# Optimization experiments

Measured on AMD Instinct MI355X. Metric: run time of the kernel, lower is better.

Reference implementation:

```python
import jax, jax.numpy as jnp
import numpy as np

N_PAIRS = 100000
N_TRIP = 500000
PAIR_DIM = 128
GEOM_DIM = 4


def _mlp(x, w1, b1, w2, b2):
    return jax.nn.silu(x @ w1 + b1) @ w2 + b2


def setup_inputs() -> dict:
    key = jax.random.key(0)
    ks = jax.random.split(key, 16)

    def lin(k, fan_in, fan_out):
        bound = 1.0 / np.sqrt(fan_in)
        kw, kb = jax.random.split(k)
        w = jax.random.uniform(kw, (fan_in, fan_out), jnp.float32, -bound, bound)
        b = jax.random.uniform(kb, (fan_out,), jnp.float32, -bound, bound)
        return w, b

    psi_w1, psi_b1 = lin(ks[0], 3 * PAIR_DIM + GEOM_DIM, PAIR_DIM)
    psi_w2, psi_b2 = lin(ks[1], PAIR_DIM, PAIR_DIM)
    phi_w1, phi_b1 = lin(ks[2], 2 * PAIR_DIM, PAIR_DIM)
    phi_w2, phi_b2 = lin(ks[3], PAIR_DIM, PAIR_DIM)

    return {
        "h_pair": jax.random.normal(ks[4], (N_PAIRS, PAIR_DIM), jnp.float32),
        "pair_vu_idx": jax.random.randint(ks[5], (N_TRIP,), 0, N_PAIRS, jnp.int64 if jax.config.jax_enable_x64 else jnp.int32).astype(jnp.int32),
        "pair_uw_idx": jax.random.randint(ks[6], (N_TRIP,), 0, N_PAIRS).astype(jnp.int32),
        "pair_vw_idx": jax.random.randint(ks[7], (N_TRIP,), 0, N_PAIRS).astype(jnp.int32),
        "geom_features": jax.random.normal(ks[8], (N_TRIP, GEOM_DIM), jnp.float32),
        "psi_w1": psi_w1, "psi_b1": psi_b1, "psi_w2": psi_w2, "psi_b2": psi_b2,
        "phi_w1": phi_w1, "phi_b1": phi_b1, "phi_w2": phi_w2, "phi_b2": phi_b2,
    }


def reference(h_pair, pair_vu_idx, pair_uw_idx, pair_vw_idx, geom_features,
              psi_w1, psi_b1, psi_w2, psi_b2,
              phi_w1, phi_b1, phi_w2, phi_b2):
    # gather triplet endpoints: [T, pair_dim] each
    h_vu = h_pair[pair_vu_idx]
    h_uw = h_pair[pair_uw_idx]
    h_vw = h_pair[pair_vw_idx]
    triplet_input = jnp.concatenate([h_vu, h_uw, h_vw, geom_features], axis=-1)  # [T, 3D+G]
    m_triplet = _mlp(triplet_input, psi_w1, psi_b1, psi_w2, psi_b2)  # [T, D]
    # scatter-add back onto pairs indexed by vw
    agg = jax.ops.segment_sum(m_triplet, pair_vw_idx, num_segments=h_pair.shape[0])  # [N, D]
    updated = _mlp(jnp.concatenate([h_pair, agg], axis=-1), phi_w1, phi_b1, phi_w2, phi_b2)
    return h_pair + updated
```

## Files before the change

kernel.cpp:

```cpp
#include <hip/hip_runtime.h>
#include <hip/hip_bf16.h>

#define T_TRIP 500000
#define NP     100000
#define NTILES 7813

typedef float f32x4 __attribute__((ext_vector_type(4)));
typedef __bf16 bf16x8 __attribute__((ext_vector_type(8)));
typedef unsigned short u16;
typedef unsigned short u16x8 __attribute__((ext_vector_type(8)));

__device__ __forceinline__ u16 f2bf(float f) {
  union { float f; unsigned u; } v; v.f = f;
  unsigned r = v.u + 0x7fffu + ((v.u >> 16) & 1u);
  return (u16)(r >> 16);
}

__device__ __forceinline__ ushort4 cvt4(float4 v) {
  ushort4 o; o.x = f2bf(v.x); o.y = f2bf(v.y); o.z = f2bf(v.z); o.w = f2bf(v.w);
  return o;
}

#define MFMA16(a, b, c) __builtin_amdgcn_mfma_f32_16x16x32_bf16((a), (b), (c), 0, 0, 0)

#define WAITVM(N) asm volatile("s_waitcnt vmcnt(" #N ")" ::: "memory")
#define LGKM0()   asm volatile("s_waitcnt lgkmcnt(0)" ::: "memory")

__device__ __forceinline__ void barrier_raw() {
  asm volatile("" ::: "memory");
  __builtin_amdgcn_s_barrier();
  asm volatile("" ::: "memory");
  __builtin_amdgcn_sched_barrier(0);
}

__device__ __forceinline__ void gload_lds16(const u16* g, u16* l) {
  __builtin_amdgcn_global_load_lds((const __attribute__((address_space(1))) void*)g,
                                   (__attribute__((address_space(3))) void*)l, 16, 0, 0);
}
__device__ __forceinline__ void gload_lds4(const int* g, int* l) {
  __builtin_amdgcn_global_load_lds((const __attribute__((address_space(1))) void*)g,
                                   (__attribute__((address_space(3))) void*)l, 4, 0, 0);
}

#define FP_W1A   0u
#define FP_W1B   16384u
#define FP_W1C   32768u
#define FP_W2    49152u
#define FP_PW1   65536u
#define FP_PW2   98304u
#define FP_W1D   114688u
#define FP_H     131072u
#define FP_AGG   12931072u
#define WS_NEED_BYTES 51462144ull

#define HSTR  136
#define GSTR  520
#define X2STR 264

__global__ void k_prep_fast(const float* __restrict__ psi_w1, const float* __restrict__ psi_w2,
                            const float* __restrict__ phi_w1, const float* __restrict__ phi_w2,
                            u16* __restrict__ ws) {
  int i = blockIdx.x * 256 + threadIdx.x;
  if (i < 49152) {
    int s = i / 16384, r = i % 16384;
    int n = r / 128, k = r % 128;
    ws[FP_W1A + i] = f2bf(psi_w1[(s * 128 + k) * 128 + n]);
    return;
  }
  i -= 49152;
  if (i < 16384) {
    int n = i / 128, k = i % 128;
    ws[FP_W2 + i] = f2bf(psi_w2[k * 128 + n]);
    return;
  }
  i -= 16384;
  if (i < 32768) {
    int n = i / 256, k = i % 256;
    ws[FP_PW1 + i] = f2bf(phi_w1[k * 128 + n]);
    return;
  }
  i -= 32768;
  if (i < 16384) {
    int n = i / 128, k = i % 128;
    ws[FP_PW2 + i] = f2bf(phi_w2[k * 128 + n]);
    return;
  }
  i -= 16384;
  if (i < 512) {
    int k = i / 128, n = i % 128;
    reinterpret_cast<float*>(ws + FP_W1D)[i] = psi_w1[(384 + k) * 128 + n];
  }
}

__global__ void k_hconv(const float* __restrict__ h, u16* __restrict__ H, u16* __restrict__ AGG) {
  const size_t i = (size_t)(blockIdx.x * 256 + threadIdx.x) * 8;
  float4 v0 = *reinterpret_cast<const float4*>(h + i);
  float4 v1 = *reinterpret_cast<const float4*>(h + i + 4);
  *reinterpret_cast<ushort4*>(H + i)     = cvt4(v0);
  *reinterpret_cast<ushort4*>(H + i + 4) = cvt4(v1);
  ushort4 z = {0, 0, 0, 0};
  *reinterpret_cast<ushort4*>(AGG + i)     = z;
  *reinterpret_cast<ushort4*>(AGG + i + 4) = z;
}

__global__ __launch_bounds__(256, 3) void k_triplet_fast(
    const u16* __restrict__ H,
    const int* __restrict__ ivu, const int* __restrict__ iuw, const int* __restrict__ ivw,
    const float* __restrict__ geom,
    const u16* __restrict__ W1A, const u16* __restrict__ W1B, const u16* __restrict__ W1C,
    const float* __restrict__ w1dF, const u16* __restrict__ W2T,
    const float* __restrict__ b1, const float* __restrict__ b2,
    u16* __restrict__ AGG) {
  __shared__ __align__(16) u16 XB[2][16 * GSTR];
  __shared__ __align__(16) u16 hl[64 * HSTR];
  __shared__ __align__(16) float geomF[2][64][4];
  __shared__ int svw[2][64];

  const int tid = threadIdx.x;
  const int w = tid >> 6, l = tid & 63;
  const int lr = l & 15;
  const int lk = (l >> 4) << 3;
  const int n0 = w * 32 + lr;
  const int rowh = (l >> 4) << 2;
  const int srow = l >> 4;
  const int schunk = (l & 15) ^ ((l >> 4) << 1);

  bf16x8 w2f[4][2];
#pragma unroll
  for (int ks = 0; ks < 4; ++ks)
#pragma unroll
    for (int ct = 0; ct < 2; ++ct)
      w2f[ks][ct] = *reinterpret_cast<const bf16x8*>(&W2T[(size_t)(n0 + ct * 16) * 128 + ks * 32 + lk]);
  const float b1v[2] = {b1[n0], b1[n0 + 16]};
  const float b2v[2] = {b2[n0], b2[n0 + 16]};
  float w1dv[4][2];
#pragma unroll
  for (int k = 0; k < 4; ++k) {
    w1dv[k][0] = w1dF[k * 128 + n0];
    w1dv[k][1] = w1dF[k * 128 + n0 + 16];
  }

  auto stage_src = [&](const int* idxa, int tile, int buf) {
    const int t0 = tile * 64;
#pragma unroll
    for (int q = 0; q < 4; ++q) {
      const int g = w * 4 + q;
      int t = t0 + g * 4 + srow; t = (t < T_TRIP) ? t : (T_TRIP - 1);
      const int idx = idxa[t];
      gload_lds16(H + (size_t)idx * 128 + schunk * 8, &XB[buf][g * GSTR]);
    }
  };

  auto stage_aux = [&](int tile, int tb) {
    const int t0 = tile * 64;
    int t = t0 + l; t = (t < T_TRIP) ? t : (T_TRIP - 1);
    if (w == 0) {
      gload_lds16(reinterpret_cast<const u16*>(geom + (size_t)t * 4),
                  reinterpret_cast<u16*>(&geomF[tb][0][0]));
    } else if (w == 1) {
      gload_lds4(ivw + t, &svw[tb][0]);
    }
  };

  auto gemm_src = [&](const u16* WT, int buf, f32x4 (&acc)[4][2]) {
#pragma unroll
    for (int ks = 0; ks < 4; ++ks) {
      bf16x8 a[4], b[2];
#pragma unroll
      for (int rt = 0; rt < 4; ++rt) {
        const int r = rt * 16 + lr;
        const int g = r >> 2, s = r & 3;
        const int j = ks * 4 + (l >> 4);
        a[rt] = *reinterpret_cast<const bf16x8*>(&XB[buf][g * GSTR + s * 128 + ((j ^ (s << 1)) << 3)]);
      }
#pragma unroll
      for (int ct = 0; ct < 2; ++ct)
        b[ct] = *reinterpret_cast<const bf16x8*>(&WT[(size_t)(n0 + ct * 16) * 128 + ks * 32 + lk]);
#pragma unroll
      for (int rt = 0; rt < 4; ++rt)
#pragma unroll
        for (int ct = 0; ct < 2; ++ct)
          acc[rt][ct] = MFMA16(a[rt], b[ct], acc[rt][ct]);
    }
  };

  int pb = 0, tb = 0;
  int tt = blockIdx.x;
  stage_src(ivu, tt, 0);

  for (; tt < NTILES; tt += gridDim.x) {
    const int t0 = tt * 64;
    int ttn = tt + gridDim.x; if (ttn >= NTILES) ttn = tt;

    stage_src(iuw, tt, pb ^ 1);
    stage_aux(tt, tb);
    WAITVM(4);
    barrier_raw();

    f32x4 acc[4][2] = {};
    gemm_src(W1A, pb, acc);
    barrier_raw();

    stage_src(ivw, tt, pb);
    WAITVM(4);
    barrier_raw();

    gemm_src(W1B, pb ^ 1, acc);

    WAITVM(0);
    barrier_raw();

    stage_src(ivu, ttn, pb ^ 1);
    gemm_src(W1C, pb, acc);

#pragma unroll
    for (int rt = 0; rt < 4; ++rt)
#pragma unroll
      for (int j = 0; j < 4; ++j) {
        const float4 g4 = *reinterpret_cast<const float4*>(&geomF[tb][rt * 16 + rowh + j][0]);
#pragma unroll
        for (int ct = 0; ct < 2; ++ct)
          acc[rt][ct][j] += g4.x * w1dv[0][ct] + g4.y * w1dv[1][ct] +
                            g4.z * w1dv[2][ct] + g4.w * w1dv[3][ct];
      }

#pragma unroll
    for (int rt = 0; rt < 4; ++rt)
#pragma unroll
      for (int ct = 0; ct < 2; ++ct) {
        const float bb = b1v[ct];
#pragma unroll
        for (int j = 0; j < 4; ++j) {
          float v = acc[rt][ct][j] + bb;
          v = v / (1.f + __expf(-v));
          hl[(rt * 16 + rowh + j) * HSTR + n0 + ct * 16] = f2bf(v);
        }
      }
    LGKM0();
    barrier_raw();

    f32x4 acc2[4][2] = {};
#pragma unroll
    for (int ks = 0; ks < 4; ++ks) {
      bf16x8 a[4];
#pragma unroll
      for (int rt = 0; rt < 4; ++rt)
        a[rt] = *reinterpret_cast<const bf16x8*>(&hl[(rt * 16 + lr) * HSTR + ks * 32 + lk]);
#pragma unroll
      for (int rt = 0; rt < 4; ++rt)
#pragma unroll
        for (int ct = 0; ct < 2; ++ct)
          acc2[rt][ct] = MFMA16(a[rt], w2f[ks][ct], acc2[rt][ct]);
    }

#pragma unroll
    for (int rt = 0; rt < 4; ++rt) {
      const int4 d4 = *reinterpret_cast<const int4*>(&svw[tb][rt * 16 + rowh]);
#pragma unroll
      for (int j = 0; j < 4; ++j) {
        const int dst = (&d4.x)[j];
        const int trow = t0 + rt * 16 + rowh + j;
        float v0 = acc2[rt][0][j] + b2v[0];
        float v1 = acc2[rt][1][j] + b2v[1];
        float x0 = __shfl_xor(v0, 1, 64);
        float x1 = __shfl_xor(v1, 1, 64);
        const bool even = (l & 1) == 0;
        float lo = even ? v0 : x1;
        float hi = even ? x0 : v1;
        const int col = even ? n0 : (n0 + 15);
        if (trow < T_TRIP) {
          u16* p = AGG + (size_t)dst * 128 + col;
          unsigned pk = ((unsigned)f2bf(hi) << 16) | (unsigned)f2bf(lo);
          asm volatile("global_atomic_pk_add_bf16 %0, %1, off" :: "v"(p), "v"(pk) : "memory");
        }
      }
    }
    pb ^= 1; tb ^= 1;
  }
  WAITVM(0);
}

__global__ __launch_bounds__(256, 3) void k_pair_fast(
    const float* __restrict__ h_pair, const u16* __restrict__ H, const u16* __restrict__ AGG,
    const u16* __restrict__ PW1T, const u16* __restrict__ PW2T,
    const float* __restrict__ b1, const float* __restrict__ b2,
    float* __restrict__ out) {
  __shared__ __align__(16) u16 xl[64 * X2STR];
  __shared__ __align__(16) u16 hl[64 * HSTR];

  const int tid = threadIdx.x;
  const int r0 = blockIdx.x * 64;

  {
    const int row = tid >> 2, q = tid & 3;
    int rc = r0 + row; rc = (rc < NP) ? rc : (NP - 1);
    const u16x8* sh = reinterpret_cast<const u16x8*>(H + (size_t)rc * 128 + q * 32);
    const u16x8* sa = reinterpret_cast<const u16x8*>(AGG + (size_t)rc * 128 + q * 32);
    u16x8* d1 = reinterpret_cast<u16x8*>(&xl[row * X2STR + q * 32]);
    u16x8* d2 = reinterpret_cast<u16x8*>(&xl[row * X2STR + 128 + q * 32]);
#pragma unroll
    for (int i = 0; i < 4; ++i) { d1[i] = sh[i]; d2[i] = sa[i]; }
  }
  __syncthreads();

  const int w = tid >> 6, l = tid & 63;
  const int lr = l & 15;
  const int lk = (l >> 4) << 3;
  const int n0 = w * 32 + lr;
  const int rowh = (l >> 4) << 2;

  f32x4 acc[4][2] = {};
#pragma unroll 1
  for (int ks = 0; ks < 8; ++ks) {
    const int k0 = ks * 32;
    bf16x8 a[4], b[2];
#pragma unroll
    for (int rt = 0; rt < 4; ++rt)
      a[rt] = *reinterpret_cast<const bf16x8*>(&xl[(rt * 16 + lr) * X2STR + k0 + lk]);
#pragma unroll
    for (int ct = 0; ct < 2; ++ct)
      b[ct] = *reinterpret_cast<const bf16x8*>(&PW1T[(size_t)(n0 + ct * 16) * 256 + k0 + lk]);
#pragma unroll
    for (int rt = 0; rt < 4; ++rt)
#pragma unroll
      for (int ct = 0; ct < 2; ++ct)
        acc[rt][ct] = MFMA16(a[rt], b[ct], acc[rt][ct]);
  }

  {
    const float b1v0 = b1[n0], b1v1 = b1[n0 + 16];
#pragma unroll
    for (int rt = 0; rt < 4; ++rt)
#pragma unroll
      for (int ct = 0; ct < 2; ++ct) {
        const float bb = ct ? b1v1 : b1v0;
#pragma unroll
        for (int j = 0; j < 4; ++j) {
          float v = acc[rt][ct][j] + bb;
          v = v / (1.f + __expf(-v));
          hl[(rt * 16 + rowh + j) * HSTR + n0 + ct * 16] = f2bf(v);
        }
      }
  }
  __syncthreads();

  f32x4 acc2[4][2] = {};
#pragma unroll
  for (int ks = 0; ks < 4; ++ks) {
    const int k0 = ks * 32;
    bf16x8 a[4], b[2];
#pragma unroll
    for (int rt = 0; rt < 4; ++rt)
      a[rt] = *reinterpret_cast<const bf16x8*>(&hl[(rt * 16 + lr) * HSTR + k0 + lk]);
#pragma unroll
    for (int ct = 0; ct < 2; ++ct)
      b[ct] = *reinterpret_cast<const bf16x8*>(&PW2T[(size_t)(n0 + ct * 16) * 128 + k0 + lk]);
#pragma unroll
    for (int rt = 0; rt < 4; ++rt)
#pragma unroll
      for (int ct = 0; ct < 2; ++ct)
        acc2[rt][ct] = MFMA16(a[rt], b[ct], acc2[rt][ct]);
  }

  {
    const float b2v0 = b2[n0], b2v1 = b2[n0 + 16];
#pragma unroll
    for (int rt = 0; rt < 4; ++rt)
#pragma unroll
      for (int j = 0; j < 4; ++j) {
        const int row = rt * 16 + rowh + j;
        const int r = r0 + row;
        if (r < NP) {
          out[(size_t)r * 128 + n0]      = h_pair[(size_t)r * 128 + n0]      + acc2[rt][0][j] + b2v0;
          out[(size_t)r * 128 + n0 + 16] = h_pair[(size_t)r * 128 + n0 + 16] + acc2[rt][1][j] + b2v1;
        }
      }
  }
}

#define PSI_W1T_OFF 0
#define PSI_W2T_OFF 53248
#define PHI_W1T_OFF 69632
#define PHI_W2T_OFF 102400
#define WS_U16_TOTAL 118784
#define XSTR 424

__global__ void k_prep(const float* __restrict__ psi_w1, const float* __restrict__ psi_w2,
                       const float* __restrict__ phi_w1, const float* __restrict__ phi_w2,
                       u16* __restrict__ ws) {
  int i = blockIdx.x * 256 + threadIdx.x;
  if (i < 128 * 416) {
    int n = i / 416, k = i % 416;
    ws[PSI_W1T_OFF + i] = f2bf(k < 388 ? psi_w1[k * 128 + n] : 0.f);
    return;
  }
  i -= 128 * 416;
  if (i < 128 * 128) {
    int n = i / 128, k = i % 128;
    ws[PSI_W2T_OFF + i] = f2bf(psi_w2[k * 128 + n]);
    return;
  }
  i -= 128 * 128;
  if (i < 128 * 256) {
    int n = i / 256, k = i % 256;
    ws[PHI_W1T_OFF + i] = f2bf(phi_w1[k * 128 + n]);
    return;
  }
  i -= 128 * 256;
  if (i < 128 * 128) {
    int n = i / 128, k = i % 128;
    ws[PHI_W2T_OFF + i] = f2bf(phi_w2[k * 128 + n]);
  }
}

__global__ __launch_bounds__(256, 2) void k_triplet(
    const float* __restrict__ h_pair,
    const int* __restrict__ ivu, const int* __restrict__ iuw, const int* __restrict__ ivw,
    const float* __restrict__ geom,
    const u16* __restrict__ W1T, const u16* __restrict__ W2T,
    const float* __restrict__ b1, const float* __restrict__ b2,
    float* __restrict__ agg) {
  __shared__ __align__(16) u16 xl[64 * XSTR];
  __shared__ __align__(16) u16 hl[64 * HSTR];
  __shared__ int svw[64];

  const int tid = threadIdx.x;
  const int t0 = blockIdx.x * 64;

  {
    const int row = tid >> 2, q = tid & 3;
    const int t = t0 + row;
    const int tc = (t < T_TRIP) ? t : (T_TRIP - 1);
    if (q == 0) svw[row] = (t < T_TRIP) ? ivw[tc] : -1;
    int idx[3];
    idx[0] = ivu[tc]; idx[1] = iuw[tc]; idx[2] = ivw[tc];
#pragma unroll
    for (int s = 0; s < 3; ++s) {
      const float4* src = reinterpret_cast<const float4*>(h_pair + (size_t)idx[s] * 128 + q * 32);
      u16* dst = &xl[row * XSTR + s * 128 + q * 32];
#pragma unroll
      for (int i = 0; i < 8; ++i)
        *reinterpret_cast<ushort4*>(dst + i * 4) = cvt4(src[i]);
    }
  }
  if (tid < 64) {
    const int t = t0 + tid;
    const int tc = (t < T_TRIP) ? t : (T_TRIP - 1);
    const float4 g = reinterpret_cast<const float4*>(geom)[tc];
    u16* dst = &xl[tid * XSTR + 384];
    *reinterpret_cast<ushort4*>(dst) = cvt4(g);
    ushort4 z = {0, 0, 0, 0};
#pragma unroll
    for (int i = 1; i < 8; ++i) *reinterpret_cast<ushort4*>(dst + i * 4) = z;
  }
  __syncthreads();

  const int w = tid >> 6;
  const int l = tid & 63;
  const int lr = l & 15;
  const int lk = (l >> 4) << 3;
  const int n0 = w * 32 + lr;
  const int rowh = (l >> 4) << 2;

  f32x4 acc[4][2] = {};
#pragma unroll 1
  for (int ks = 0; ks < 13; ++ks) {
    const int k0 = ks * 32;
    bf16x8 a[4], b[2];
#pragma unroll
    for (int rt = 0; rt < 4; ++rt)
      a[rt] = *reinterpret_cast<const bf16x8*>(&xl[(rt * 16 + lr) * XSTR + k0 + lk]);
#pragma unroll
    for (int ct = 0; ct < 2; ++ct)
      b[ct] = *reinterpret_cast<const bf16x8*>(&W1T[(size_t)(n0 + ct * 16) * 416 + k0 + lk]);
#pragma unroll
    for (int rt = 0; rt < 4; ++rt)
#pragma unroll
      for (int ct = 0; ct < 2; ++ct)
        acc[rt][ct] = MFMA16(a[rt], b[ct], acc[rt][ct]);
  }

  {
    const float b1v0 = b1[n0], b1v1 = b1[n0 + 16];
#pragma unroll
    for (int rt = 0; rt < 4; ++rt)
#pragma unroll
      for (int ct = 0; ct < 2; ++ct) {
        const float bb = ct ? b1v1 : b1v0;
#pragma unroll
        for (int j = 0; j < 4; ++j) {
          float v = acc[rt][ct][j] + bb;
          v = v / (1.f + __expf(-v));
          hl[(rt * 16 + rowh + j) * HSTR + n0 + ct * 16] = f2bf(v);
        }
      }
  }
  __syncthreads();

  f32x4 acc2[4][2] = {};
#pragma unroll
  for (int ks = 0; ks < 4; ++ks) {
    const int k0 = ks * 32;
    bf16x8 a[4], b[2];
#pragma unroll
    for (int rt = 0; rt < 4; ++rt)
      a[rt] = *reinterpret_cast<const bf16x8*>(&hl[(rt * 16 + lr) * HSTR + k0 + lk]);
#pragma unroll
    for (int ct = 0; ct < 2; ++ct)
      b[ct] = *reinterpret_cast<const bf16x8*>(&W2T[(size_t)(n0 + ct * 16) * 128 + k0 + lk]);
#pragma unroll
    for (int rt = 0; rt < 4; ++rt)
#pragma unroll
      for (int ct = 0; ct < 2; ++ct)
        acc2[rt][ct] = MFMA16(a[rt], b[ct], acc2[rt][ct]);
  }

  {
    const float b2v0 = b2[n0], b2v1 = b2[n0 + 16];
#pragma unroll
    for (int rt = 0; rt < 4; ++rt)
#pragma unroll
      for (int j = 0; j < 4; ++j) {
        const int row = rt * 16 + rowh + j;
        const int dst = svw[row];
        if (dst >= 0) {
          unsafeAtomicAdd(&agg[(size_t)dst * 128 + n0], acc2[rt][0][j] + b2v0);
          unsafeAtomicAdd(&agg[(size_t)dst * 128 + n0 + 16], acc2[rt][1][j] + b2v1);
        }
      }
  }
}

__global__ __launch_bounds__(256, 2) void k_pair(
    const float* __restrict__ h_pair,
    const u16* __restrict__ W1T, const u16* __restrict__ W2T,
    const float* __restrict__ b1, const float* __restrict__ b2,
    float* __restrict__ out) {
  __shared__ __align__(16) u16 xl[64 * X2STR];
  __shared__ __align__(16) u16 hl[64 * HSTR];

  const int tid = threadIdx.x;
  const int r0 = blockIdx.x * 64;

  {
    const int row = tid >> 2, q = tid & 3;
    const int r = r0 + row;
    const int rc = (r < NP) ? r : (NP - 1);
    const float4* s1 = reinterpret_cast<const float4*>(h_pair + (size_t)rc * 128 + q * 32);
    const float4* s2 = reinterpret_cast<const float4*>(out + (size_t)rc * 128 + q * 32);
    u16* d1 = &xl[row * X2STR + q * 32];
    u16* d2 = &xl[row * X2STR + 128 + q * 32];
#pragma unroll
    for (int i = 0; i < 8; ++i) {
      *reinterpret_cast<ushort4*>(d1 + i * 4) = cvt4(s1[i]);
      *reinterpret_cast<ushort4*>(d2 + i * 4) = cvt4(s2[i]);
    }
  }
  __syncthreads();

  const int w = tid >> 6;
  const int l = tid & 63;
  const int lr = l & 15;
  const int lk = (l >> 4) << 3;
  const int n0 = w * 32 + lr;
  const int rowh = (l >> 4) << 2;

  f32x4 acc[4][2] = {};
#pragma unroll 1
  for (int ks = 0; ks < 8; ++ks) {
    const int k0 = ks * 32;
    bf16x8 a[4], b[2];
#pragma unroll
    for (int rt = 0; rt < 4; ++rt)
      a[rt] = *reinterpret_cast<const bf16x8*>(&xl[(rt * 16 + lr) * X2STR + k0 + lk]);
#pragma unroll
    for (int ct = 0; ct < 2; ++ct)
      b[ct] = *reinterpret_cast<const bf16x8*>(&W1T[(size_t)(n0 + ct * 16) * 256 + k0 + lk]);
#pragma unroll
    for (int rt = 0; rt < 4; ++rt)
#pragma unroll
      for (int ct = 0; ct < 2; ++ct)
        acc[rt][ct] = MFMA16(a[rt], b[ct], acc[rt][ct]);
  }

  {
    const float b1v0 = b1[n0], b1v1 = b1[n0 + 16];
#pragma unroll
    for (int rt = 0; rt < 4; ++rt)
#pragma unroll
      for (int ct = 0; ct < 2; ++ct) {
        const float bb = ct ? b1v1 : b1v0;
#pragma unroll
        for (int j = 0; j < 4; ++j) {
          float v = acc[rt][ct][j] + bb;
          v = v / (1.f + __expf(-v));
          hl[(rt * 16 + rowh + j) * HSTR + n0 + ct * 16] = f2bf(v);
        }
      }
  }
  __syncthreads();

  f32x4 acc2[4][2] = {};
#pragma unroll
  for (int ks = 0; ks < 4; ++ks) {
    const int k0 = ks * 32;
    bf16x8 a[4], b[2];
#pragma unroll
    for (int rt = 0; rt < 4; ++rt)
      a[rt] = *reinterpret_cast<const bf16x8*>(&hl[(rt * 16 + lr) * HSTR + k0 + lk]);
#pragma unroll
    for (int ct = 0; ct < 2; ++ct)
      b[ct] = *reinterpret_cast<const bf16x8*>(&W2T[(size_t)(n0 + ct * 16) * 128 + k0 + lk]);
#pragma unroll
    for (int rt = 0; rt < 4; ++rt)
#pragma unroll
      for (int ct = 0; ct < 2; ++ct)
        acc2[rt][ct] = MFMA16(a[rt], b[ct], acc2[rt][ct]);
  }

  {
    const float b2v0 = b2[n0], b2v1 = b2[n0 + 16];
#pragma unroll
    for (int rt = 0; rt < 4; ++rt)
#pragma unroll
      for (int j = 0; j < 4; ++j) {
        const int row = rt * 16 + rowh + j;
        const int r = r0 + row;
        if (r < NP) {
          out[(size_t)r * 128 + n0]      = h_pair[(size_t)r * 128 + n0]      + acc2[rt][0][j] + b2v0;
          out[(size_t)r * 128 + n0 + 16] = h_pair[(size_t)r * 128 + n0 + 16] + acc2[rt][1][j] + b2v1;
        }
      }
  }
}

extern "C" void kernel_launch(void* const* d_in, const int* in_sizes, int n_in,
                              void* d_out, int out_size, void* d_ws, size_t ws_size,
                              hipStream_t stream) {
  const float* h_pair = (const float*)d_in[0];
  const int* ivu = (const int*)d_in[1];
  const int* iuw = (const int*)d_in[2];
  const int* ivw = (const int*)d_in[3];
  const float* geom = (const float*)d_in[4];
  const float* psi_w1 = (const float*)d_in[5];
  const float* psi_b1 = (const float*)d_in[6];
  const float* psi_w2 = (const float*)d_in[7];
  const float* psi_b2 = (const float*)d_in[8];
  const float* phi_w1 = (const float*)d_in[9];
  const float* phi_b1 = (const float*)d_in[10];
  const float* phi_w2 = (const float*)d_in[11];
  const float* phi_b2 = (const float*)d_in[12];

  float* out = (float*)d_out;
  u16* ws = (u16*)d_ws;

  if (ws_size >= WS_NEED_BYTES) {
    k_prep_fast<<<450, 256, 0, stream>>>(psi_w1, psi_w2, phi_w1, phi_w2, ws);
    k_hconv<<<6250, 256, 0, stream>>>(h_pair, ws + FP_H, ws + FP_AGG);
    k_triplet_fast<<<768, 256, 0, stream>>>(
        ws + FP_H, ivu, iuw, ivw, geom,
        ws + FP_W1A, ws + FP_W1B, ws + FP_W1C,
        reinterpret_cast<const float*>(ws + FP_W1D), ws + FP_W2,
        psi_b1, psi_b2, ws + FP_AGG);
    k_pair_fast<<<(NP + 63) / 64, 256, 0, stream>>>(
        h_pair, ws + FP_H, ws + FP_AGG,
        ws + FP_PW1, ws + FP_PW2, phi_b1, phi_b2, out);
  } else {
    hipMemsetAsync(d_out, 0, (size_t)out_size * sizeof(float), stream);
    k_prep<<<(WS_U16_TOTAL + 255) / 256, 256, 0, stream>>>(psi_w1, psi_w2, phi_w1, phi_w2, ws);
    k_triplet<<<(T_TRIP + 63) / 64, 256, 0, stream>>>(
        h_pair, ivu, iuw, ivw, geom,
        ws + PSI_W1T_OFF, ws + PSI_W2T_OFF, psi_b1, psi_b2, out);
    k_pair<<<(NP + 63) / 64, 256, 0, stream>>>(
        h_pair, ws + PHI_W1T_OFF, ws + PHI_W2T_OFF, phi_b1, phi_b2, out);
  }
}
```

Baseline: 279.8 us.

## Prefetch triplet indices into LDS and defer scatter atomics by one tile

The triplet kernel now stages the ivu/iuw/ivw index arrays and geometry into LDS one tile ahead through async global-to-LDS loads, so the gather address computation reads indices from LDS instead of issuing dependent global loads. The bf16 atomic scatter of each tile's output is deferred and issued after the next tile's first-layer GEMMs, overlapping atomic latency with MFMA work. SiLU now uses a hardware reciprocal, and bf16 conversion uses the packed cvt instruction in both kernels. This adds register pressure from the carried accumulators and destination indices, plus an extra full vmcnt wait and barrier per tile.

```diff
diff --git a/kernel.cpp b/kernel.cpp
--- a/kernel.cpp
+++ b/kernel.cpp
@@ -19,6 +19,12 @@
 __device__ __forceinline__ ushort4 cvt4(float4 v) {
   ushort4 o; o.x = f2bf(v.x); o.y = f2bf(v.y); o.z = f2bf(v.z); o.w = f2bf(v.w);
   return o;
+}
+
+__device__ __forceinline__ u16 cvt1_pk(float v) {
+  unsigned r;
+  asm("v_cvt_pk_bf16_f32 %0, %1, %1" : "=v"(r) : "v"(v));
+  return (u16)r;
 }
 
 #define MFMA16(a, b, c) __builtin_amdgcn_mfma_f32_16x16x32_bf16((a), (b), (c), 0, 0, 0)
@@ -113,8 +119,10 @@
     u16* __restrict__ AGG) {
   __shared__ __align__(16) u16 XB[2][16 * GSTR];
   __shared__ __align__(16) u16 hl[64 * HSTR];
-  __shared__ __align__(16) float geomF[2][64][4];
-  __shared__ int svw[2][64];
+  __shared__ __align__(16) float geomF[64][4];
+  __shared__ __align__(16) int aIvu[2][64];
+  __shared__ __align__(16) int aIuw[64];
+  __shared__ __align__(16) int svw[2][64];
 
   const int tid = threadIdx.x;
   const int w = tid >> 6, l = tid & 63;
@@ -140,25 +148,29 @@
     w1dv[k][1] = w1dF[k * 128 + n0 + 16];
   }
 
-  auto stage_src = [&](const int* idxa, int tile, int buf) {
-    const int t0 = tile * 64;
+  auto stage_src_lds = [&](const int* idxL, int buf) {
 #pragma unroll
     for (int q = 0; q < 4; ++q) {
       const int g = w * 4 + q;
-      int t = t0 + g * 4 + srow; t = (t < T_TRIP) ? t : (T_TRIP - 1);
-      const int idx = idxa[t];
+      const int idx = idxL[g * 4 + srow];
       gload_lds16(H + (size_t)idx * 128 + schunk * 8, &XB[buf][g * GSTR]);
     }
   };
 
-  auto stage_aux = [&](int tile, int tb) {
-    const int t0 = tile * 64;
-    int t = t0 + l; t = (t < T_TRIP) ? t : (T_TRIP - 1);
+  auto stage_aux = [&](int tn, int tn2, int buf) {
     if (w == 0) {
+      int t = tn2 * 64 + l; t = (t < T_TRIP) ? t : (T_TRIP - 1);
+      gload_lds4(ivu + t, &aIvu[buf][0]);
+    } else if (w == 1) {
+      int t = tn * 64 + l; t = (t < T_TRIP) ? t : (T_TRIP - 1);
+      gload_lds4(iuw + t, &aIuw[0]);
+    } else if (w == 2) {
+      int t = tn * 64 + l; t = (t < T_TRIP) ? t : (T_TRIP - 1);
+      gload_lds4(ivw + t, &svw[buf][0]);
+    } else {
+      int t = tn * 64 + l; t = (t < T_TRIP) ? t : (T_TRIP - 1);
       gload_lds16(reinterpret_cast<const u16*>(geom + (size_t)t * 4),
-                  reinterpret_cast<u16*>(&geomF[tb][0][0]));
-    } else if (w == 1) {
-      gload_lds4(ivw + t, &svw[tb][0]);
+                  reinterpret_cast<u16*>(&geomF[0][0]));
     }
   };
 
@@ -184,99 +196,149 @@
     }
   };
 
-  int pb = 0, tb = 0;
-  int tt = blockIdx.x;
-  stage_src(ivu, tt, 0);
-
-  for (; tt < NTILES; tt += gridDim.x) {
-    const int t0 = tt * 64;
-    int ttn = tt + gridDim.x; if (ttn >= NTILES) ttn = tt;
-
-    stage_src(iuw, tt, pb ^ 1);
-    stage_aux(tt, tb);
-    WAITVM(4);
-    barrier_raw();
-
-    f32x4 acc[4][2] = {};
-    gemm_src(W1A, pb, acc);
-    barrier_raw();
-
-    stage_src(ivw, tt, pb);
-    WAITVM(4);
-    barrier_raw();
-
-    gemm_src(W1B, pb ^ 1, acc);
-
-    WAITVM(0);
-    barrier_raw();
-
-    stage_src(ivu, ttn, pb ^ 1);
-    gemm_src(W1C, pb, acc);
-
-#pragma unroll
-    for (int rt = 0; rt < 4; ++rt)
+  int4 dst4[4];
+  f32x4 acc2c[4][2];
+#pragma unroll
+  for (int rt = 0; rt < 4; ++rt) {
+    dst4[rt] = make_int4(-1, -1, -1, -1);
+#pragma unroll
+    for (int ct = 0; ct < 2; ++ct) acc2c[rt][ct] = f32x4{0.f, 0.f, 0.f, 0.f};
+  }
+
+  auto scatter_prev = [&]() {
+#pragma unroll
+    for (int rt = 0; rt < 4; ++rt) {
 #pragma unroll
       for (int j = 0; j < 4; ++j) {
-        const float4 g4 = *reinterpret_cast<const float4*>(&geomF[tb][rt * 16 + rowh + j][0]);
-#pragma unroll
-        for (int ct = 0; ct < 2; ++ct)
-          acc[rt][ct][j] += g4.x * w1dv[0][ct] + g4.y * w1dv[1][ct] +
-                            g4.z * w1dv[2][ct] + g4.w * w1dv[3][ct];
-      }
-
-#pragma unroll
-    for (int rt = 0; rt < 4; ++rt)
-#pragma unroll
-      for (int ct = 0; ct < 2; ++ct) {
-        const float bb = b1v[ct];
-#pragma unroll
-        for (int j = 0; j < 4; ++j) {
-          float v = acc[rt][ct][j] + bb;
-          v = v / (1.f + __expf(-v));
-          hl[(rt * 16 + rowh + j) * HSTR + n0 + ct * 16] = f2bf(v);
-        }
-      }
-    LGKM0();
-    barrier_raw();
-
-    f32x4 acc2[4][2] = {};
-#pragma unroll
-    for (int ks = 0; ks < 4; ++ks) {
-      bf16x8 a[4];
-#pragma unroll
-      for (int rt = 0; rt < 4; ++rt)
-        a[rt] = *reinterpret_cast<const bf16x8*>(&hl[(rt * 16 + lr) * HSTR + ks * 32 + lk]);
-#pragma unroll
-      for (int rt = 0; rt < 4; ++rt)
-#pragma unroll
-        for (int ct = 0; ct < 2; ++ct)
-          acc2[rt][ct] = MFMA16(a[rt], w2f[ks][ct], acc2[rt][ct]);
-    }
-
-#pragma unroll
-    for (int rt = 0; rt < 4; ++rt) {
-      const int4 d4 = *reinterpret_cast<const int4*>(&svw[tb][rt * 16 + rowh]);
-#pragma unroll
-      for (int j = 0; j < 4; ++j) {
-        const int dst = (&d4.x)[j];
-        const int trow = t0 + rt * 16 + rowh + j;
-        float v0 = acc2[rt][0][j] + b2v[0];
-        float v1 = acc2[rt][1][j] + b2v[1];
-        float x0 = __shfl_xor(v0, 1, 64);
-        float x1 = __shfl_xor(v1, 1, 64);
+        const int dst = (&dst4[rt].x)[j];
+        float v0 = acc2c[rt][0][j];
+        float v1 = acc2c[rt][1][j];
+        float x0 = __shfl_xor(v0, 1);
+        float x1 = __shfl_xor(v1, 1);
         const bool even = (l & 1) == 0;
         float lo = even ? v0 : x1;
         float hi = even ? x0 : v1;
         const int col = even ? n0 : (n0 + 15);
-        if (trow < T_TRIP) {
+        if (dst >= 0) {
           u16* p = AGG + (size_t)dst * 128 + col;
-          unsigned pk = ((unsigned)f2bf(hi) << 16) | (unsigned)f2bf(lo);
+          unsigned pk;
+          asm("v_cvt_pk_bf16_f32 %0, %1, %2" : "=v"(pk) : "v"(lo), "v"(hi));
           asm volatile("global_atomic_pk_add_bf16 %0, %1, off" :: "v"(p), "v"(pk) : "memory");
         }
       }
     }
+  };
+
+  int pb = 0, tb = 0;
+  int tt = blockIdx.x;
+  const int G = gridDim.x;
+
+  {
+    int tn2 = (tt + G < NTILES) ? tt + G : tt;
+    stage_aux(tt, tn2, 0);
+#pragma unroll
+    for (int q = 0; q < 4; ++q) {
+      const int g = w * 4 + q;
+      int t = tt * 64 + g * 4 + srow; t = (t < T_TRIP) ? t : (T_TRIP - 1);
+      const int idx = ivu[t];
+      gload_lds16(H + (size_t)idx * 128 + schunk * 8, &XB[0][g * GSTR]);
+    }
+    WAITVM(0);
+    barrier_raw();
+  }
+
+  for (; tt < NTILES; tt += G) {
+    const int t0 = tt * 64;
+
+    stage_src_lds(aIuw, pb ^ 1);
+    WAITVM(4);
+    barrier_raw();
+
+    f32x4 acc[4][2] = {};
+    gemm_src(W1A, pb, acc);
+    barrier_raw();
+
+    int4 nd[4];
+#pragma unroll
+    for (int rt = 0; rt < 4; ++rt)
+      nd[rt] = *reinterpret_cast<const int4*>(&svw[tb][rt * 16 + rowh]);
+    stage_src_lds(&svw[tb][0], pb);
+    WAITVM(4);
+    barrier_raw();
+
+    gemm_src(W1B, pb ^ 1, acc);
+    WAITVM(0);
+    barrier_raw();
+
+    stage_src_lds(&aIvu[tb][0], pb ^ 1);
+
+    gemm_src(W1C, pb, acc);
+
+    scatter_prev();
+
+#pragma unroll
+    for (int rt = 0; rt < 4; ++rt)
+#pragma unroll
+      for (int j = 0; j < 4; ++j) {
+        const float4 g4 = *reinterpret_cast<const float4*>(&geomF[rt * 16 + rowh + j][0]);
+#pragma unroll
+        for (int ct = 0; ct < 2; ++ct)
+          acc[rt][ct][j] += g4.x * w1dv[0][ct] + g4.y * w1dv[1][ct] +
+                            g4.z * w1dv[2][ct] + g4.w * w1dv[3][ct];
+      }
+#pragma unroll
+    for (int rt = 0; rt < 4; ++rt)
+#pragma unroll
+      for (int ct = 0; ct < 2; ++ct) {
+        const float bb = b1v[ct];
+#pragma unroll
+        for (int j = 0; j < 4; ++j) {
+          float v = acc[rt][ct][j] + bb;
+          v = v * __builtin_amdgcn_rcpf(1.f + __expf(-v));
+          hl[(rt * 16 + rowh + j) * HSTR + n0 + ct * 16] = cvt1_pk(v);
+        }
+      }
+    LGKM0();
+    barrier_raw();
+
+    {
+      int tn = (tt + G < NTILES) ? tt + G : tt;
+      int tn2 = (tt + 2 * G < NTILES) ? tt + 2 * G : tt;
+      stage_aux(tn, tn2, tb ^ 1);
+    }
+
+    f32x4 acc2[4][2] = {};
+#pragma unroll
+    for (int ks = 0; ks < 4; ++ks) {
+      bf16x8 a[4];
+#pragma unroll
+      for (int rt = 0; rt < 4; ++rt)
+        a[rt] = *reinterpret_cast<const bf16x8*>(&hl[(rt * 16 + lr) * HSTR + ks * 32 + lk]);
+#pragma unroll
+      for (int rt = 0; rt < 4; ++rt)
+#pragma unroll
+        for (int ct = 0; ct < 2; ++ct)
+          acc2[rt][ct] = MFMA16(a[rt], w2f[ks][ct], acc2[rt][ct]);
+    }
+
+#pragma unroll
+    for (int rt = 0; rt < 4; ++rt) {
+#pragma unroll
+      for (int j = 0; j < 4; ++j) {
+        const int trow = t0 + rt * 16 + rowh + j;
+        (&dst4[rt].x)[j] = (trow < T_TRIP) ? (&nd[rt].x)[j] : -1;
+      }
+#pragma unroll
+      for (int ct = 0; ct < 2; ++ct)
+        acc2c[rt][ct] = acc2[rt][ct] + b2v[ct];
+    }
+
+    WAITVM(0);
+    barrier_raw();
     pb ^= 1; tb ^= 1;
   }
+
+  scatter_prev();
   WAITVM(0);
 }
 
@@ -337,8 +399,8 @@
 #pragma unroll
         for (int j = 0; j < 4; ++j) {
           float v = acc[rt][ct][j] + bb;
-          v = v / (1.f + __expf(-v));
-          hl[(rt * 16 + rowh + j) * HSTR + n0 + ct * 16] = f2bf(v);
+          v = v * __builtin_amdgcn_rcpf(1.f + __expf(-v));
+          hl[(rt * 16 + rowh + j) * HSTR + n0 + ct * 16] = cvt1_pk(v);
         }
       }
   }
```

New measurement: 299.3 us. 6.9% more time.
